# Performance work log

Hardware: AMD Instinct MI355X
Metric: run time of the kernel (lower is better)

The kernel has to match this reference:

```python
import jax, jax.numpy as jnp
import numpy as np


def _sobel_filters():
    # fil is the 3x3 smoothing kernel [[1,2,1],[2,4,2],[1,2,1]]
    fil = np.array([[1, 2, 1], [2, 4, 2], [1, 2, 1]], dtype=np.float32)
    fx = np.zeros((3, 3, 3), dtype=np.float32)
    fx[0, :, :] = fil
    fx[2, :, :] = -fil
    fy = np.zeros((3, 3, 3), dtype=np.float32)
    fy[:, 0, :] = fil
    fy[:, 2, :] = -fil
    fz = np.zeros((3, 3, 3), dtype=np.float32)
    fz[:, :, 0] = fil
    fz[:, :, 2] = -fil
    # Stack the three fixed (non-learned) filters as 3 output channels: [O=3, I=1, 3,3,3]
    return jnp.asarray(np.stack([fx, fy, fz])[:, None])


_FILT = _sobel_filters()
_DN = ('NCDHW', 'OIDHW', 'NCDHW')


def _grad3d(v):
    # v: [N,1,D,H,W] -> [N,3,D,H,W], padding=1 == SAME for 3x3x3 stride 1
    return jax.lax.conv_general_dilated(
        v, _FILT.astype(v.dtype), window_strides=(1, 1, 1),
        padding='SAME', dimension_numbers=_DN)


def setup_inputs() -> dict:
    key = jax.random.key(0)
    k1, k2 = jax.random.split(key)
    shape = (2, 1, 160, 192, 224)
    x = jax.random.normal(k1, shape, dtype=jnp.float32)
    y = jax.random.normal(k2, shape, dtype=jnp.float32)
    return {"x": x, "y": y}


def reference(x, y):
    gx = _grad3d(x)  # [N,3,D,H,W]
    gy = _grad3d(y)
    d2 = (gx - gy) ** 2
    # sum over the 3 directions of the per-direction MSE
    return jnp.sum(jnp.mean(d2, axis=(0, 2, 3, 4)))
```

## Files before the change

kernel.cpp:

```cpp
#include <hip/hip_runtime.h>
#include <stdint.h>


#define N_  2
#define D_  160
#define H_  192
#define W_  224
#define PS  (H_ * W_)

#define TD  10
#define RW  4
#define TH  8
constexpr float SCALE = 1.0f / ((float)N_ * D_ * H_ * W_);

__device__ __forceinline__ float4 f4add(float4 a, float4 b) {
    return make_float4(a.x + b.x, a.y + b.y, a.z + b.z, a.w + b.w);
}
__device__ __forceinline__ float4 f4sub(float4 a, float4 b) {
    return make_float4(a.x - b.x, a.y - b.y, a.z - b.z, a.w - b.w);
}
__device__ __forceinline__ float4 f4fma(float k, float4 a, float4 b) {
    return make_float4(fmaf(k, a.x, b.x), fmaf(k, a.y, b.y),
                       fmaf(k, a.z, b.z), fmaf(k, a.w, b.w));
}

#define LOADP(p, XR) do {                                                      \
    int pc_ = min(max((p), 0), D_ - 1);              \
    const float* bx_ = vbx + (size_t)pc_ * PS;                                 \
    const float* by_ = vby + (size_t)pc_ * PS;                                 \
    _Pragma("unroll")                                                          \
    for (int r_ = 0; r_ < 6; ++r_) {                                           \
        XR[2 * r_]     = *(const float4*)(bx_ + off[r_]);                      \
        XR[2 * r_ + 1] = *(const float4*)(by_ + off[r_]);                      \
    }                                                                          \
} while (0)

#define BODY(ITV, XR) do {                                                     \
    const int it_ = (ITV);                                                     \
    const int q_ = d0 - 1 + it_;                 \
    const float pm_ = (q_ >= 0 && q_ < D_) ? 1.f : 0.f;                        \
    float4 n0[RW], n1[RW], n2[RW];                                             \
    _Pragma("unroll")                                                          \
    for (int r_ = 0; r_ < 6; ++r_) {                                           \
        const float m_ = rmask[r_] * pm_;                                      \
        const float4 vv = make_float4((XR[2*r_].x - XR[2*r_+1].x) * m_,        \
                                      (XR[2*r_].y - XR[2*r_+1].y) * m_,        \
                                      (XR[2*r_].z - XR[2*r_+1].z) * m_,        \
                                      (XR[2*r_].w - XR[2*r_+1].w) * m_);       \
        float Lm = __shfl_up(vv.w, 1, 64);                                     \
        float Rp = __shfl_down(vv.x, 1, 64);                                   \
        if (lane == 0) Lm = 0.f;                          \
                    \
        const float4 s_ = make_float4(Lm + 2.f * vv.x + vv.y,                  \
                                      vv.x + 2.f * vv.y + vv.z,                \
                                      vv.y + 2.f * vv.z + vv.w,                \
                                      vv.z + 2.f * vv.w + Rp);                 \
        const float4 g_ = make_float4(Lm - vv.y, vv.x - vv.z,                  \
                                      vv.y - vv.w, vv.z - Rp);                 \
        _Pragma("unroll")                                                      \
        for (int j_ = 0; j_ < RW; ++j_) {                                      \
            if (r_ == j_) {                           \
                n0[j_] = s_; n1[j_] = s_; n2[j_] = g_;                         \
            } else if (r_ == j_ + 1) {               \
                n0[j_] = f4fma(2.f, s_, n0[j_]);                               \
                n2[j_] = f4fma(2.f, g_, n2[j_]);                               \
            } else if (r_ == j_ + 2) {                         \
                n0[j_] = f4add(n0[j_], s_);                                    \
                n1[j_] = f4sub(n1[j_], s_);                                    \
                n2[j_] = f4add(n2[j_], g_);                                    \
            }                                                                  \
        }                                                                      \
    }                                                                          \
            \
    if (it_ < TD) LOADP(d0 + 1 + it_, XR);                                     \
                 \
    if (it_ >= 2 && wact) {                                                    \
        _Pragma("unroll")                                                      \
        for (int j_ = 0; j_ < RW; ++j_) {                                      \
            const float4 gx = f4sub(A0[j_], n0[j_]);                           \
            const float4 gy = f4add(f4fma(2.f, B1[j_], A1[j_]), n1[j_]);       \
            const float4 gz = f4add(f4fma(2.f, B2[j_], A2[j_]), n2[j_]);       \
            acc = fmaf(gx.x, gx.x, acc); acc = fmaf(gx.y, gx.y, acc);          \
            acc = fmaf(gx.z, gx.z, acc); acc = fmaf(gx.w, gx.w, acc);          \
            acc = fmaf(gy.x, gy.x, acc); acc = fmaf(gy.y, gy.y, acc);          \
            acc = fmaf(gy.z, gy.z, acc); acc = fmaf(gy.w, gy.w, acc);          \
            acc = fmaf(gz.x, gz.x, acc); acc = fmaf(gz.y, gz.y, acc);          \
            acc = fmaf(gz.z, gz.z, acc); acc = fmaf(gz.w, gz.w, acc);          \
        }                                                                      \
    }                                                                          \
                                                           \
    _Pragma("unroll")                                                          \
    for (int j_ = 0; j_ < RW; ++j_) {                                          \
        A0[j_] = B0[j_]; A1[j_] = B1[j_]; A2[j_] = B2[j_];                     \
        B0[j_] = n0[j_]; B1[j_] = n1[j_]; B2[j_] = n2[j_];                     \
    }                                                                          \
} while (0)

__global__ __launch_bounds__(128, 1)
void grad_loss_kernel(const float* __restrict__ x, const float* __restrict__ y,
                      float* __restrict__ out) {
    __shared__ float wsum[2];

    const int tid  = threadIdx.x;
    const int lane = tid & 63;
    const int wv   = tid >> 6;

    const int nchunks = D_ / TD;
    const int nb = blockIdx.z / nchunks;
    const int d0 = (blockIdx.z % nchunks) * TD;
    const int h0w = blockIdx.y * TH + RW * wv;

    const float* vbx = x + (size_t)nb * ((size_t)D_ * PS);
    const float* vby = y + (size_t)nb * ((size_t)D_ * PS);

    const bool wact = lane < 56;
    const int lo4c = (lane < 56 ? lane : 55) * 4;
    int off[6];
    float rmask[6];
    #pragma unroll
    for (int r = 0; r < 6; ++r) {
        int gh  = h0w - 1 + r;
        int ghc = min(max(gh, 0), H_ - 1);
        off[r]   = ghc * W_ + lo4c;
        rmask[r] = (((unsigned)gh < (unsigned)H_) && wact) ? 1.f : 0.f;
    }

    float4 XRa[12], XRb[12];

    float4 A0[RW], A1[RW], A2[RW], B0[RW], B1[RW], B2[RW];
    const float4 z4 = make_float4(0.f, 0.f, 0.f, 0.f);
    #pragma unroll
    for (int j = 0; j < RW; ++j) { A0[j]=A1[j]=A2[j]=B0[j]=B1[j]=B2[j]=z4; }
    float acc = 0.f;

    LOADP(d0 - 1, XRa);
    LOADP(d0,     XRb);

    #pragma unroll 1
    for (int i2 = 0; i2 < (TD + 2) / 2; ++i2) {
        BODY(2 * i2,     XRa);
        BODY(2 * i2 + 1, XRb);
    }

    #pragma unroll
    for (int off_ = 32; off_ > 0; off_ >>= 1)
        acc += __shfl_xor(acc, off_, 64);
    if (lane == 0) wsum[wv] = acc;
    __syncthreads();
    if (tid == 0) {
        atomicAdd(out, (wsum[0] + wsum[1]) * SCALE);
    }
}

extern "C" void kernel_launch(void* const* d_in, const int* in_sizes, int n_in,
                              void* d_out, int out_size, void* d_ws, size_t ws_size,
                              hipStream_t stream) {
    const float* x = (const float*)d_in[0];
    const float* y = (const float*)d_in[1];
    float* out = (float*)d_out;

    hipMemsetAsync(out, 0, sizeof(float), stream);

    dim3 block(128);
    dim3 grid(1,
              H_ / TH,
              N_ * (D_ / TD));
    grad_loss_kernel<<<grid, block, 0, stream>>>(x, y, out);
}
```

Measured before the change: 136.7 us.

## Split width into two overlapping float2 segments with single-wave blocks

Each lane now handles two columns via float2 loads instead of four via float4, and the 224-wide row is covered by two overlapping 114-column segments in separate blocks along grid x. Blocks shrink to a single wave, covering 4 rows instead of 8, which removes shared memory and the block barrier, and each wave does its own atomicAdd. This raises the number of waves and the memory-level parallelism of a bandwidth-bound stencil. The cost is narrower loads, some redundant halo columns loaded across segments, and four times as many atomics.

```diff
diff --git a/kernel.cpp b/kernel.cpp
--- a/kernel.cpp
+++ b/kernel.cpp
@@ -10,18 +10,16 @@
 
 #define TD  10
 #define RW  4
-#define TH  8
 constexpr float SCALE = 1.0f / ((float)N_ * D_ * H_ * W_);
 
-__device__ __forceinline__ float4 f4add(float4 a, float4 b) {
-    return make_float4(a.x + b.x, a.y + b.y, a.z + b.z, a.w + b.w);
+__device__ __forceinline__ float2 f2add(float2 a, float2 b) {
+    return make_float2(a.x + b.x, a.y + b.y);
 }
-__device__ __forceinline__ float4 f4sub(float4 a, float4 b) {
-    return make_float4(a.x - b.x, a.y - b.y, a.z - b.z, a.w - b.w);
+__device__ __forceinline__ float2 f2sub(float2 a, float2 b) {
+    return make_float2(a.x - b.x, a.y - b.y);
 }
-__device__ __forceinline__ float4 f4fma(float k, float4 a, float4 b) {
-    return make_float4(fmaf(k, a.x, b.x), fmaf(k, a.y, b.y),
-                       fmaf(k, a.z, b.z), fmaf(k, a.w, b.w));
+__device__ __forceinline__ float2 f2fma(float k, float2 a, float2 b) {
+    return make_float2(fmaf(k, a.x, b.x), fmaf(k, a.y, b.y));
 }
 
 #define LOADP(p, XR) do {                                                      \
@@ -30,8 +28,8 @@
     const float* by_ = vby + (size_t)pc_ * PS;                                 \
     _Pragma("unroll")                                                          \
     for (int r_ = 0; r_ < 6; ++r_) {                                           \
-        XR[2 * r_]     = *(const float4*)(bx_ + off[r_]);                      \
-        XR[2 * r_ + 1] = *(const float4*)(by_ + off[r_]);                      \
+        XR[2 * r_]     = *(const float2*)(bx_ + off[r_]);                      \
+        XR[2 * r_ + 1] = *(const float2*)(by_ + off[r_]);                      \
     }                                                                          \
 } while (0)
 
@@ -39,53 +37,46 @@
     const int it_ = (ITV);                                                     \
     const int q_ = d0 - 1 + it_;                 \
     const float pm_ = (q_ >= 0 && q_ < D_) ? 1.f : 0.f;                        \
-    float4 n0[RW], n1[RW], n2[RW];                                             \
+    float2 n0[RW], n1[RW], n2[RW];                                             \
     _Pragma("unroll")                                                          \
     for (int r_ = 0; r_ < 6; ++r_) {                                           \
         const float m_ = rmask[r_] * pm_;                                      \
-        const float4 vv = make_float4((XR[2*r_].x - XR[2*r_+1].x) * m_,        \
-                                      (XR[2*r_].y - XR[2*r_+1].y) * m_,        \
-                                      (XR[2*r_].z - XR[2*r_+1].z) * m_,        \
-                                      (XR[2*r_].w - XR[2*r_+1].w) * m_);       \
-        float Lm = __shfl_up(vv.w, 1, 64);                                     \
+        const float2 vv = make_float2((XR[2*r_].x - XR[2*r_+1].x) * m_,        \
+                                      (XR[2*r_].y - XR[2*r_+1].y) * m_);       \
+        float Lm = __shfl_up(vv.y, 1, 64);                                     \
         float Rp = __shfl_down(vv.x, 1, 64);                                   \
-        if (lane == 0) Lm = 0.f;                          \
-                    \
-        const float4 s_ = make_float4(Lm + 2.f * vv.x + vv.y,                  \
-                                      vv.x + 2.f * vv.y + vv.z,                \
-                                      vv.y + 2.f * vv.z + vv.w,                \
-                                      vv.z + 2.f * vv.w + Rp);                 \
-        const float4 g_ = make_float4(Lm - vv.y, vv.x - vv.z,                  \
-                                      vv.y - vv.w, vv.z - Rp);                 \
+        if (lane == 0) Lm = 0.f;    \
+         \
+                       \
+        const float2 s_ = make_float2(Lm + 2.f * vv.x + vv.y,                  \
+                                      vv.x + 2.f * vv.y + Rp);                 \
+        const float2 g_ = make_float2(Lm - vv.y, vv.x - Rp);                   \
         _Pragma("unroll")                                                      \
         for (int j_ = 0; j_ < RW; ++j_) {                                      \
             if (r_ == j_) {                           \
                 n0[j_] = s_; n1[j_] = s_; n2[j_] = g_;                         \
             } else if (r_ == j_ + 1) {               \
-                n0[j_] = f4fma(2.f, s_, n0[j_]);                               \
-                n2[j_] = f4fma(2.f, g_, n2[j_]);                               \
+                n0[j_] = f2fma(2.f, s_, n0[j_]);                               \
+                n2[j_] = f2fma(2.f, g_, n2[j_]);                               \
             } else if (r_ == j_ + 2) {                         \
-                n0[j_] = f4add(n0[j_], s_);                                    \
-                n1[j_] = f4sub(n1[j_], s_);                                    \
-                n2[j_] = f4add(n2[j_], g_);                                    \
+                n0[j_] = f2add(n0[j_], s_);                                    \
+                n1[j_] = f2sub(n1[j_], s_);                                    \
+                n2[j_] = f2add(n2[j_], g_);                                    \
             }                                                                  \
         }                                                                      \
     }                                                                          \
             \
     if (it_ < TD) LOADP(d0 + 1 + it_, XR);                                     \
                  \
-    if (it_ >= 2 && wact) {                                                    \
+    if (it_ >= 2 && omask) {                                                   \
         _Pragma("unroll")                                                      \
         for (int j_ = 0; j_ < RW; ++j_) {                                      \
-            const float4 gx = f4sub(A0[j_], n0[j_]);                           \
-            const float4 gy = f4add(f4fma(2.f, B1[j_], A1[j_]), n1[j_]);       \
-            const float4 gz = f4add(f4fma(2.f, B2[j_], A2[j_]), n2[j_]);       \
+            const float2 gx = f2sub(A0[j_], n0[j_]);                           \
+            const float2 gy = f2add(f2fma(2.f, B1[j_], A1[j_]), n1[j_]);       \
+            const float2 gz = f2add(f2fma(2.f, B2[j_], A2[j_]), n2[j_]);       \
             acc = fmaf(gx.x, gx.x, acc); acc = fmaf(gx.y, gx.y, acc);          \
-            acc = fmaf(gx.z, gx.z, acc); acc = fmaf(gx.w, gx.w, acc);          \
             acc = fmaf(gy.x, gy.x, acc); acc = fmaf(gy.y, gy.y, acc);          \
-            acc = fmaf(gy.z, gy.z, acc); acc = fmaf(gy.w, gy.w, acc);          \
             acc = fmaf(gz.x, gz.x, acc); acc = fmaf(gz.y, gz.y, acc);          \
-            acc = fmaf(gz.z, gz.z, acc); acc = fmaf(gz.w, gz.w, acc);          \
         }                                                                      \
     }                                                                          \
                                                            \
@@ -96,41 +87,41 @@
     }                                                                          \
 } while (0)
 
-__global__ __launch_bounds__(128, 1)
+__global__ __launch_bounds__(64, 1)
 void grad_loss_kernel(const float* __restrict__ x, const float* __restrict__ y,
                       float* __restrict__ out) {
-    __shared__ float wsum[2];
+    const int lane = threadIdx.x;
 
-    const int tid  = threadIdx.x;
-    const int lane = tid & 63;
-    const int wv   = tid >> 6;
-
+    const int seg = blockIdx.x;
+    const int h0w = blockIdx.y * RW;
     const int nchunks = D_ / TD;
     const int nb = blockIdx.z / nchunks;
     const int d0 = (blockIdx.z % nchunks) * TD;
-    const int h0w = blockIdx.y * TH + RW * wv;
 
     const float* vbx = x + (size_t)nb * ((size_t)D_ * PS);
     const float* vby = y + (size_t)nb * ((size_t)D_ * PS);
 
-    const bool wact = lane < 56;
-    const int lo4c = (lane < 56 ? lane : 55) * 4;
+    const int lc = min(lane, 56);
+    const int base_w = (seg == 0) ? 2 * lc : 110 + 2 * lc;
+    const float lmask = (lane <= 56) ? 1.f : 0.f;
+    const bool omask = (seg == 0) ? (lane < 56) : (lane >= 1 && lane < 57);
+
     int off[6];
     float rmask[6];
     #pragma unroll
     for (int r = 0; r < 6; ++r) {
         int gh  = h0w - 1 + r;
         int ghc = min(max(gh, 0), H_ - 1);
-        off[r]   = ghc * W_ + lo4c;
-        rmask[r] = (((unsigned)gh < (unsigned)H_) && wact) ? 1.f : 0.f;
+        off[r]   = ghc * W_ + base_w;
+        rmask[r] = (((unsigned)gh < (unsigned)H_)) ? lmask : 0.f;
     }
 
-    float4 XRa[12], XRb[12];
+    float2 XRa[12], XRb[12];
 
-    float4 A0[RW], A1[RW], A2[RW], B0[RW], B1[RW], B2[RW];
-    const float4 z4 = make_float4(0.f, 0.f, 0.f, 0.f);
+    float2 A0[RW], A1[RW], A2[RW], B0[RW], B1[RW], B2[RW];
+    const float2 z2 = make_float2(0.f, 0.f);
     #pragma unroll
-    for (int j = 0; j < RW; ++j) { A0[j]=A1[j]=A2[j]=B0[j]=B1[j]=B2[j]=z4; }
+    for (int j = 0; j < RW; ++j) { A0[j]=A1[j]=A2[j]=B0[j]=B1[j]=B2[j]=z2; }
     float acc = 0.f;
 
     LOADP(d0 - 1, XRa);
@@ -145,11 +136,7 @@
     #pragma unroll
     for (int off_ = 32; off_ > 0; off_ >>= 1)
         acc += __shfl_xor(acc, off_, 64);
-    if (lane == 0) wsum[wv] = acc;
-    __syncthreads();
-    if (tid == 0) {
-        atomicAdd(out, (wsum[0] + wsum[1]) * SCALE);
-    }
+    if (lane == 0) atomicAdd(out, acc * SCALE);
 }
 
 extern "C" void kernel_launch(void* const* d_in, const int* in_sizes, int n_in,
@@ -161,9 +148,9 @@
 
     hipMemsetAsync(out, 0, sizeof(float), stream);
 
-    dim3 block(128);
-    dim3 grid(1,
-              H_ / TH,
+    dim3 block(64);
+    dim3 grid(2,
+              H_ / RW,
               N_ * (D_ / TD));
     grad_loss_kernel<<<grid, block, 0, stream>>>(x, y, out);
 }
```

New measurement: 159.9 us. 1.17x slower.
